# Optimization experiments

Hardware: AMD Instinct MI355X
Metric: run time of the kernel (lower is better)

The kernel has to match this reference:

```python
import jax, jax.numpy as jnp
import numpy as np

B, L, D = 32, 2048, 128
SCALE = 1.0 / float(np.sqrt(D))  # scale = 1/sqrt(dim_K) per docstring


def setup_inputs() -> dict:
    key = jax.random.key(0)
    kq, kk, kv, kb = jax.random.split(key, 4)
    return {
        "Q": jax.random.normal(kq, (B, L, D), dtype=jnp.float32),
        "K": jax.random.normal(kk, (B, L, D), dtype=jnp.float32),
        "V": jax.random.normal(kv, (B, L, D), dtype=jnp.float32),
        "bias": jax.random.normal(kb, (L, L), dtype=jnp.float32),
    }


def reference(Q, K, V, bias):
    # scores = Q @ K^T + bias (bias broadcast over batch), then scale, softmax, @ V
    scores = jnp.einsum("bqd,bkd->bqk", Q, K) + bias[None, :, :]
    attn = jax.nn.softmax(scores * SCALE, axis=-1)  # [B, L, L]
    context = jnp.einsum("bqk,bkd->bqd", attn, V)   # [B, L, D]
    return (context, attn[0])
```

## Files before the change

### kernel.cpp

```cpp
#include <hip/hip_runtime.h>
#include <cstdint>
#include <cstddef>

#define L_ 2048
#define D_ 128
#define B_ 32
#define NT_ 32

static constexpr float SCALE = 0.08838834764831845f;
static constexpr float LOG2E = 1.4426950408889634f;
static constexpr float THR_  = 8.0f;

typedef __bf16 bf16x8 __attribute__((ext_vector_type(8)));
typedef __bf16 bf16x4 __attribute__((ext_vector_type(4)));
typedef float  f32x4  __attribute__((ext_vector_type(4)));
typedef int    i32x4  __attribute__((ext_vector_type(4)));

typedef const __attribute__((address_space(1))) uint32_t* gas_t;
typedef __attribute__((address_space(3))) uint32_t*       las_t;

__device__ __forceinline__ void dma16(const void* g, void* l) {
  __builtin_amdgcn_global_load_lds((gas_t)g, (las_t)l, 16, 0, 0);
}

__global__ __launch_bounds__(256) void prep_kv(
    const float* __restrict__ K, const float* __restrict__ V,
    __bf16* __restrict__ gK, __bf16* __restrict__ gVt)
{
  const int b   = blockIdx.x >> 5;
  const int kt  = blockIdx.x & 31;
  const int tid = threadIdx.x;
  const size_t tile = ((size_t)b * NT_ + kt) * 8192;

#pragma unroll
  for (int i = 0; i < 4; ++i) {
    const int g  = tid + i * 256;
    const int r  = g >> 4;
    const int c  = g & 15;
    const int d0 = (c ^ (r & 7)) * 8;
    const float* src = K + ((size_t)b * L_ + kt * 64 + r) * D_ + d0;
    float4 a = *(const float4*)src;
    float4 e = *(const float4*)(src + 4);
    bf16x8 f;
    f[0]=(__bf16)a.x; f[1]=(__bf16)a.y; f[2]=(__bf16)a.z; f[3]=(__bf16)a.w;
    f[4]=(__bf16)e.x; f[5]=(__bf16)e.y; f[6]=(__bf16)e.z; f[7]=(__bf16)e.w;
    *(bf16x8*)((char*)(gK + tile) + r * 256 + c * 16) = f;
  }

  __shared__ alignas(16) __bf16 Vt[8192];
  char* vb = (char*)Vt;
  const int vr     = tid & 63;
  const int vdbase = (tid >> 6) * 32;
  const float* vrow = V + ((size_t)b * L_ + kt * 64 + vr) * D_ + vdbase;
#pragma unroll
  for (int c = 0; c < 8; ++c) {
    float4 v4 = *(const float4*)(vrow + c * 4);
    const int d0 = vdbase + c * 4;
    float vv[4] = {v4.x, v4.y, v4.z, v4.w};
#pragma unroll
    for (int jj = 0; jj < 4; ++jj) {
      const int d = d0 + jj;
      *(__bf16*)(vb + d * 128 + ((vr * 2) ^ ((d & 7) << 4))) = (__bf16)vv[jj];
    }
  }
  __syncthreads();
#pragma unroll
  for (int i = 0; i < 4; ++i) {
    const int off = (tid + i * 256) * 16;
    *(i32x4*)((char*)(gVt + tile) + off) = *(const i32x4*)(vb + off);
  }
}

__global__ __launch_bounds__(256) void prep_bias(
    const float* __restrict__ bias, float* __restrict__ biasS)
{
#pragma unroll
  for (int it = 0; it < 4; ++it) {
    const size_t idx = ((size_t)it * 1024 + blockIdx.x) * 256 + threadIdx.x;
    float4 v = ((const float4*)bias)[idx];
    v.x *= SCALE; v.y *= SCALE; v.z *= SCALE; v.w *= SCALE;
    ((float4*)biasS)[idx] = v;
  }
}

template<int MODE>
__global__ __launch_bounds__(512, 4) void attn_fwd(
    const float* __restrict__ Q, const float* __restrict__ K,
    const float* __restrict__ V, const float* __restrict__ bias,
    const float* __restrict__ biasS,
    const __bf16* __restrict__ gK, const __bf16* __restrict__ gVt,
    float* __restrict__ ctx, float* __restrict__ attn0)
{
  const int id   = blockIdx.x;
  const int idx  = id >> 3;
  const int b    = (id & 7) * 4 + (idx >> 4);
  const int qblk = idx & 15;

  const int tid  = threadIdx.x;
  const int wave = tid >> 6;
  const int lane = tid & 63;
  const int lg   = lane >> 4;
  const int lr   = lane & 15;

  const int qbase = qblk * 128 + wave * 16;

  __shared__ alignas(16) __bf16 Ksh[8192];
  __shared__ alignas(16) __bf16 Vtsh[8192];
  __shared__ alignas(16) __bf16 Psh[8][16 * 64];

  const char* kb = (const char*)Ksh;
  const char* vb = (const char*)Vtsh;
  char* const pw = (char*)&Psh[wave][0];

  bf16x8 qf[4];
  {
    const float* qrow = Q + ((size_t)b * L_ + (qbase + lr)) * D_;
#pragma unroll
    for (int kc = 0; kc < 4; ++kc) {
      const int d0 = kc * 32 + lg * 8;
      float4 a = *(const float4*)(qrow + d0);
      float4 c = *(const float4*)(qrow + d0 + 4);
      bf16x8 f;
      f[0] = (__bf16)(a.x * SCALE); f[1] = (__bf16)(a.y * SCALE);
      f[2] = (__bf16)(a.z * SCALE); f[3] = (__bf16)(a.w * SCALE);
      f[4] = (__bf16)(c.x * SCALE); f[5] = (__bf16)(c.y * SCALE);
      f[6] = (__bf16)(c.z * SCALE); f[7] = (__bf16)(c.w * SCALE);
      qf[kc] = f;
    }
  }

  f32x4 Oacc[8];
#pragma unroll
  for (int i = 0; i < 8; ++i) Oacc[i] = (f32x4){0.f, 0.f, 0.f, 0.f};
  float m_run = -3.0e38f;
  float lp    = 0.f;

  auto stage_dma = [&](int kt) {
    const char* gk = (const char*)(gK + ((size_t)b * NT_ + kt) * 8192);
    const char* gv = (const char*)(gVt + ((size_t)b * NT_ + kt) * 8192);
#pragma unroll
    for (int i = 0; i < 2; ++i) {
      const int off = (wave * 2 + i) * 1024;
      dma16(gk + off + lane * 16, (char*)Ksh + off);
      dma16(gv + off + lane * 16, (char*)Vtsh + off);
    }
  };

  if constexpr (MODE >= 1) stage_dma(0);

  const int sP = (lr & 3);

  for (int kt = 0; kt < NT_; ++kt) {
    const int kvbase = kt * 64;

    if constexpr (MODE == 0) {
#pragma unroll
      for (int it = 0; it < 4; ++it) {
        const int g  = tid + it * 512;
        const int r  = g >> 5;
        const int d0 = (g & 31) * 4;
        const size_t src = ((size_t)b * L_ + (kvbase + r)) * D_ + d0;
        float4 kv4 = *(const float4*)(K + src);
        bf16x4 k4 = {(__bf16)kv4.x, (__bf16)kv4.y, (__bf16)kv4.z, (__bf16)kv4.w};
        *(bf16x4*)((char*)Ksh + r * 256 + ((d0 * 2) ^ ((r & 7) << 4))) = k4;
      }
      {
        const int vr = tid & 63;
        const int vdbase = (tid >> 6) * 16;
        const float* vrow = V + ((size_t)b * L_ + (kvbase + vr)) * D_ + vdbase;
#pragma unroll
        for (int c = 0; c < 4; ++c) {
          float4 v4 = *(const float4*)(vrow + c * 4);
          const int d0 = vdbase + c * 4;
          float vv[4] = {v4.x, v4.y, v4.z, v4.w};
#pragma unroll
          for (int jj = 0; jj < 4; ++jj) {
            const int d = d0 + jj;
            *(__bf16*)((char*)Vtsh + d * 128 + ((vr * 2) ^ ((d & 7) << 4))) = (__bf16)vv[jj];
          }
        }
      }
    }
    __syncthreads();

    float4 bf4[4];
    {
      const float* bp = (MODE == 2 ? biasS : bias)
                        + (size_t)(qbase + lr) * L_ + kvbase + lg * 4;
#pragma unroll
      for (int t = 0; t < 4; ++t) bf4[t] = *(const float4*)(bp + t * 16);
    }

    f32x4 Sacc[4];
#pragma unroll
    for (int t = 0; t < 4; ++t) Sacc[t] = (f32x4){0.f, 0.f, 0.f, 0.f};
    __builtin_amdgcn_s_setprio(1);
#pragma unroll
    for (int t = 0; t < 4; ++t) {
      const int r   = t * 16 + lr;
      const int swz = (r & 7) << 4;
#pragma unroll
      for (int kc = 0; kc < 4; ++kc) {
        const int d0 = kc * 32 + lg * 8;
        bf16x8 kf = *(const bf16x8*)(kb + r * 256 + ((d0 * 2) ^ swz));
        Sacc[t] = __builtin_amdgcn_mfma_f32_16x16x32_bf16(kf, qf[kc], Sacc[t], 0, 0, 0);
      }
    }
    __builtin_amdgcn_s_setprio(0);

    float zz[4][4];
#pragma unroll
    for (int t = 0; t < 4; ++t) {
      if constexpr (MODE == 2) {
        zz[t][0] = Sacc[t][0] + bf4[t].x; zz[t][1] = Sacc[t][1] + bf4[t].y;
        zz[t][2] = Sacc[t][2] + bf4[t].z; zz[t][3] = Sacc[t][3] + bf4[t].w;
      } else {
        zz[t][0] = fmaf(bf4[t].x, SCALE, Sacc[t][0]);
        zz[t][1] = fmaf(bf4[t].y, SCALE, Sacc[t][1]);
        zz[t][2] = fmaf(bf4[t].z, SCALE, Sacc[t][2]);
        zz[t][3] = fmaf(bf4[t].w, SCALE, Sacc[t][3]);
      }
    }
    if (b == 0) {
      float* ap = attn0 + (size_t)(qbase + lr) * L_ + kvbase + lg * 4;
#pragma unroll
      for (int t = 0; t < 4; ++t)
        *(float4*)(ap + t * 16) = make_float4(zz[t][0], zz[t][1], zz[t][2], zz[t][3]);
    }

    float mt = fmaxf(fmaxf(fmaxf(zz[0][0], zz[0][1]), fmaxf(zz[0][2], zz[0][3])),
                     fmaxf(fmaxf(zz[1][0], zz[1][1]), fmaxf(zz[1][2], zz[1][3])));
    mt = fmaxf(mt, fmaxf(fmaxf(zz[2][0], zz[2][1]), fmaxf(zz[2][2], zz[2][3])));
    mt = fmaxf(mt, fmaxf(fmaxf(zz[3][0], zz[3][1]), fmaxf(zz[3][2], zz[3][3])));
    mt = fmaxf(mt, __shfl_xor(mt, 16));
    mt = fmaxf(mt, __shfl_xor(mt, 32));

    if (__any(mt > m_run + THR_)) {
      const float mnew = fmaxf(m_run, mt);
      const float corr = exp2f((m_run - mnew) * LOG2E);
      m_run = mnew;
      lp *= corr;
      float cR[4];
#pragma unroll
      for (int j = 0; j < 4; ++j)
        cR[j] = __shfl(corr, (lane & 0x30) | (lg * 4 + j));
#pragma unroll
      for (int dt = 0; dt < 8; ++dt) {
        Oacc[dt][0] *= cR[0]; Oacc[dt][1] *= cR[1];
        Oacc[dt][2] *= cR[2]; Oacc[dt][3] *= cR[3];
      }
    }

    const float mh = m_run * LOG2E;
#pragma unroll
    for (int t = 0; t < 4; ++t) {
      bf16x4 pb;
#pragma unroll
      for (int j = 0; j < 4; ++j) {
        const float p = exp2f(fmaf(zz[t][j], LOG2E, -mh));
        lp += p;
        pb[j] = (__bf16)p;
      }
      *(bf16x4*)(pw + lr * 128 + ((t ^ sP) << 5) + (lg << 3)) = pb;
    }

    __builtin_amdgcn_s_setprio(1);
#pragma unroll
    for (int kc2 = 0; kc2 < 2; ++kc2) {
      const int c0  = kc2 * 32;
      const int t_r = kc2 * 2 + (lg >> 1);
      bf16x8 pa = *(const bf16x8*)(pw + lr * 128 + ((t_r ^ sP) << 5) + ((lg & 1) << 4));
#pragma unroll
      for (int dt = 0; dt < 8; ++dt) {
        const int d = dt * 16 + lr;
        bf16x8 vf = *(const bf16x8*)(vb + d * 128 + (((c0 + lg * 8) * 2) ^ ((d & 7) << 4)));
        Oacc[dt] = __builtin_amdgcn_mfma_f32_16x16x32_bf16(pa, vf, Oacc[dt], 0, 0, 0);
      }
    }
    __builtin_amdgcn_s_setprio(0);

    __syncthreads();
    if constexpr (MODE >= 1) {
      if (kt + 1 < NT_) stage_dma(kt + 1);
    }
  }

  float ls = lp;
  ls += __shfl_xor(ls, 16);
  ls += __shfl_xor(ls, 32);
  const float linv = 1.f / ls;
  float invR[4];
#pragma unroll
  for (int j = 0; j < 4; ++j)
    invR[j] = __shfl(linv, (lane & 0x30) | (lg * 4 + j));
#pragma unroll
  for (int dt = 0; dt < 8; ++dt) {
    const int d = dt * 16 + lr;
#pragma unroll
    for (int j = 0; j < 4; ++j) {
      const int q = qbase + lg * 4 + j;
      ctx[((size_t)b * L_ + q) * D_ + d] = Oacc[dt][j] * invR[j];
    }
  }
}

__global__ __launch_bounds__(256) void softmax_rows(float* __restrict__ attn0)
{
  const int row  = blockIdx.x;
  float* p = attn0 + (size_t)row * L_;
  const int tid  = threadIdx.x;
  const int wave = tid >> 6;
  const int lane = tid & 63;
  __shared__ float red[8];

  float4 a = ((const float4*)p)[tid];
  float4 c = ((const float4*)p)[tid + 256];
  float v[8] = {a.x, a.y, a.z, a.w, c.x, c.y, c.z, c.w};

  float mx = v[0];
#pragma unroll
  for (int i = 1; i < 8; ++i) mx = fmaxf(mx, v[i]);
#pragma unroll
  for (int msk = 1; msk < 64; msk <<= 1) mx = fmaxf(mx, __shfl_xor(mx, msk));
  if (lane == 0) red[wave] = mx;
  __syncthreads();
  mx = fmaxf(fmaxf(red[0], red[1]), fmaxf(red[2], red[3]));

  float e[8];
  float s = 0.f;
#pragma unroll
  for (int i = 0; i < 8; ++i) { e[i] = exp2f((v[i] - mx) * LOG2E); s += e[i]; }
#pragma unroll
  for (int msk = 1; msk < 64; msk <<= 1) s += __shfl_xor(s, msk);
  if (lane == 0) red[4 + wave] = s;
  __syncthreads();
  s = red[4] + red[5] + red[6] + red[7];
  const float inv = 1.f / s;

  float4 o0 = {e[0] * inv, e[1] * inv, e[2] * inv, e[3] * inv};
  float4 o1 = {e[4] * inv, e[5] * inv, e[6] * inv, e[7] * inv};
  ((float4*)p)[tid]       = o0;
  ((float4*)p)[tid + 256] = o1;
}

extern "C" void kernel_launch(void* const* d_in, const int* in_sizes, int n_in,
                              void* d_out, int out_size, void* d_ws, size_t ws_size,
                              hipStream_t stream) {
  const float* Q    = (const float*)d_in[0];
  const float* K    = (const float*)d_in[1];
  const float* V    = (const float*)d_in[2];
  const float* bias = (const float*)d_in[3];
  float* ctx   = (float*)d_out;
  float* attn0 = ctx + (size_t)B_ * L_ * D_;

  const size_t kvElems  = (size_t)B_ * L_ * D_;
  const size_t needKV   = 2 * kvElems * sizeof(__bf16);
  const size_t needAll  = needKV + (size_t)L_ * L_ * sizeof(float);

  __bf16* gK    = (__bf16*)d_ws;
  __bf16* gVt   = gK + kvElems;
  float*  biasS = (float*)(gVt + kvElems);

  if (ws_size >= needAll) {
    prep_kv<<<dim3(B_ * NT_), 256, 0, stream>>>(K, V, gK, gVt);
    prep_bias<<<dim3(1024), 256, 0, stream>>>(bias, biasS);
    attn_fwd<2><<<dim3(512), 512, 0, stream>>>(Q, K, V, bias, biasS, gK, gVt, ctx, attn0);
  } else if (ws_size >= needKV) {
    prep_kv<<<dim3(B_ * NT_), 256, 0, stream>>>(K, V, gK, gVt);
    attn_fwd<1><<<dim3(512), 512, 0, stream>>>(Q, K, V, bias, nullptr, gK, gVt, ctx, attn0);
  } else {
    attn_fwd<0><<<dim3(512), 512, 0, stream>>>(Q, K, V, bias, nullptr, nullptr, nullptr, ctx, attn0);
  }
  softmax_rows<<<L_, 256, 0, stream>>>(attn0);
}
```

Before: 155.7 us.

## Double-buffer K/V tiles and keep P in registers via permuted V layout

Doubles the LDS K and V buffers so the DMA for tile kt+2 is issued while tile kt is computed, using an explicit vmcnt wait plus barrier instead of full syncs. It also drops the per-wave P shared-memory round trip: the softmax probabilities are packed straight into the MFMA A operand in registers, and a row permutation (cperm) applied to the transposed V layout makes the key order match. This removes LDS traffic and a sync on P, at the cost of double the K/V LDS footprint, which may lower occupancy. It also relies on the hand-written vmcnt count matching the number of DMAs in flight.

```diff
diff --git a/kernel.cpp b/kernel.cpp
--- a/kernel.cpp
+++ b/kernel.cpp
@@ -21,6 +21,11 @@
 
 __device__ __forceinline__ void dma16(const void* g, void* l) {
   __builtin_amdgcn_global_load_lds((gas_t)g, (las_t)l, 16, 0, 0);
+}
+
+__device__ __forceinline__ int cperm(int r) {
+  return (r & 32) | (((r >> 3) & 1) << 4) | (((r >> 2) & 1) << 3)
+       | (((r >> 4) & 1) << 2) | (r & 3);
 }
 
 __global__ __launch_bounds__(256) void prep_kv(
@@ -50,6 +55,7 @@
   __shared__ alignas(16) __bf16 Vt[8192];
   char* vb = (char*)Vt;
   const int vr     = tid & 63;
+  const int vc     = cperm(vr);
   const int vdbase = (tid >> 6) * 32;
   const float* vrow = V + ((size_t)b * L_ + kt * 64 + vr) * D_ + vdbase;
 #pragma unroll
@@ -60,7 +66,7 @@
 #pragma unroll
     for (int jj = 0; jj < 4; ++jj) {
       const int d = d0 + jj;
-      *(__bf16*)(vb + d * 128 + ((vr * 2) ^ ((d & 7) << 4))) = (__bf16)vv[jj];
+      *(__bf16*)(vb + d * 128 + ((vc * 2) ^ ((d & 7) << 4))) = (__bf16)vv[jj];
     }
   }
   __syncthreads();
@@ -104,13 +110,8 @@
 
   const int qbase = qblk * 128 + wave * 16;
 
-  __shared__ alignas(16) __bf16 Ksh[8192];
-  __shared__ alignas(16) __bf16 Vtsh[8192];
-  __shared__ alignas(16) __bf16 Psh[8][16 * 64];
-
-  const char* kb = (const char*)Ksh;
-  const char* vb = (const char*)Vtsh;
-  char* const pw = (char*)&Psh[wave][0];
+  __shared__ alignas(16) __bf16 Ksh[2 * 8192];
+  __shared__ alignas(16) __bf16 Vtsh[2 * 8192];
 
   bf16x8 qf[4];
   {
@@ -135,25 +136,33 @@
   float m_run = -3.0e38f;
   float lp    = 0.f;
 
-  auto stage_dma = [&](int kt) {
+  auto stage_dma = [&](int kt, int bufsel) {
     const char* gk = (const char*)(gK + ((size_t)b * NT_ + kt) * 8192);
     const char* gv = (const char*)(gVt + ((size_t)b * NT_ + kt) * 8192);
+    char* kdst = (char*)Ksh + bufsel * 16384;
+    char* vdst = (char*)Vtsh + bufsel * 16384;
 #pragma unroll
     for (int i = 0; i < 2; ++i) {
       const int off = (wave * 2 + i) * 1024;
-      dma16(gk + off + lane * 16, (char*)Ksh + off);
-      dma16(gv + off + lane * 16, (char*)Vtsh + off);
+      dma16(gk + off + lane * 16, kdst + off);
+      dma16(gv + off + lane * 16, vdst + off);
     }
   };
 
-  if constexpr (MODE >= 1) stage_dma(0);
-
-  const int sP = (lr & 3);
+  if constexpr (MODE >= 1) { stage_dma(0, 0); stage_dma(1, 1); }
 
   for (int kt = 0; kt < NT_; ++kt) {
     const int kvbase = kt * 64;
-
-    if constexpr (MODE == 0) {
+    const int cur = (MODE >= 1) ? (kt & 1) : 0;
+    const char* kb = (const char*)Ksh + cur * 16384;
+    const char* vb = (const char*)Vtsh + cur * 16384;
+
+    if constexpr (MODE >= 1) {
+      if (kt + 1 < NT_) asm volatile("s_waitcnt vmcnt(4)" ::: "memory");
+      else              asm volatile("s_waitcnt vmcnt(0)" ::: "memory");
+      __builtin_amdgcn_s_barrier();
+      __builtin_amdgcn_sched_barrier(0);
+    } else {
 #pragma unroll
       for (int it = 0; it < 4; ++it) {
         const int g  = tid + it * 512;
@@ -166,6 +175,7 @@
       }
       {
         const int vr = tid & 63;
+        const int vc = cperm(vr);
         const int vdbase = (tid >> 6) * 16;
         const float* vrow = V + ((size_t)b * L_ + (kvbase + vr)) * D_ + vdbase;
 #pragma unroll
@@ -176,12 +186,12 @@
 #pragma unroll
           for (int jj = 0; jj < 4; ++jj) {
             const int d = d0 + jj;
-            *(__bf16*)((char*)Vtsh + d * 128 + ((vr * 2) ^ ((d & 7) << 4))) = (__bf16)vv[jj];
+            *(__bf16*)((char*)Vtsh + d * 128 + ((vc * 2) ^ ((d & 7) << 4))) = (__bf16)vv[jj];
           }
         }
       }
-    }
-    __syncthreads();
+      __syncthreads();
+    }
 
     float4 bf4[4];
     {
@@ -251,25 +261,27 @@
       }
     }
 
+    bf16x4 pbf[4];
     const float mh = m_run * LOG2E;
 #pragma unroll
     for (int t = 0; t < 4; ++t) {
-      bf16x4 pb;
 #pragma unroll
       for (int j = 0; j < 4; ++j) {
         const float p = exp2f(fmaf(zz[t][j], LOG2E, -mh));
         lp += p;
-        pb[j] = (__bf16)p;
-      }
-      *(bf16x4*)(pw + lr * 128 + ((t ^ sP) << 5) + (lg << 3)) = pb;
+        pbf[t][j] = (__bf16)p;
+      }
     }
 
     __builtin_amdgcn_s_setprio(1);
 #pragma unroll
     for (int kc2 = 0; kc2 < 2; ++kc2) {
-      const int c0  = kc2 * 32;
-      const int t_r = kc2 * 2 + (lg >> 1);
-      bf16x8 pa = *(const bf16x8*)(pw + lr * 128 + ((t_r ^ sP) << 5) + ((lg & 1) << 4));
+      bf16x8 pa;
+      pa[0] = pbf[kc2 * 2][0];     pa[1] = pbf[kc2 * 2][1];
+      pa[2] = pbf[kc2 * 2][2];     pa[3] = pbf[kc2 * 2][3];
+      pa[4] = pbf[kc2 * 2 + 1][0]; pa[5] = pbf[kc2 * 2 + 1][1];
+      pa[6] = pbf[kc2 * 2 + 1][2]; pa[7] = pbf[kc2 * 2 + 1][3];
+      const int c0 = kc2 * 32;
 #pragma unroll
       for (int dt = 0; dt < 8; ++dt) {
         const int d = dt * 16 + lr;
@@ -279,9 +291,13 @@
     }
     __builtin_amdgcn_s_setprio(0);
 
-    __syncthreads();
     if constexpr (MODE >= 1) {
-      if (kt + 1 < NT_) stage_dma(kt + 1);
+      __builtin_amdgcn_sched_barrier(0);
+      __builtin_amdgcn_s_barrier();
+      __builtin_amdgcn_sched_barrier(0);
+      if (kt + 2 < NT_) stage_dma(kt + 2, cur);
+    } else {
+      __syncthreads();
     }
   }
 
```

After: 157.8 us. About the same (+1.3%).

## Feed P directly from registers via permuted V layout; drop bias prescale kernel

Applied to the files above, without the earlier changes.

Permutes the key-column order of the transposed V tile (in both prep_kv and the fallback path) so that the bf16 probabilities held in each lane's MFMA output registers already match the A-operand layout of the PV MFMA. This removes the per-wave LDS round trip for P: the shared-memory buffer, its stores and its reloads. The change also removes the separate prep_bias kernel and the prescaled-bias path, and folds the scale into an FMA on the raw bias inside the main loop. That saves one launch and a 16MB read and write of the bias, and frees some LDS, which could raise occupancy.

```diff
diff --git a/kernel.cpp b/kernel.cpp
--- a/kernel.cpp
+++ b/kernel.cpp
@@ -21,6 +21,11 @@
 
 __device__ __forceinline__ void dma16(const void* g, void* l) {
   __builtin_amdgcn_global_load_lds((gas_t)g, (las_t)l, 16, 0, 0);
+}
+
+__device__ __forceinline__ int cperm(int r) {
+  return (r & 32) | (((r >> 3) & 1) << 4) | (((r >> 2) & 1) << 3)
+       | (((r >> 4) & 1) << 2) | (r & 3);
 }
 
 __global__ __launch_bounds__(256) void prep_kv(
@@ -50,6 +55,7 @@
   __shared__ alignas(16) __bf16 Vt[8192];
   char* vb = (char*)Vt;
   const int vr     = tid & 63;
+  const int vc     = cperm(vr);
   const int vdbase = (tid >> 6) * 32;
   const float* vrow = V + ((size_t)b * L_ + kt * 64 + vr) * D_ + vdbase;
 #pragma unroll
@@ -60,7 +66,7 @@
 #pragma unroll
     for (int jj = 0; jj < 4; ++jj) {
       const int d = d0 + jj;
-      *(__bf16*)(vb + d * 128 + ((vr * 2) ^ ((d & 7) << 4))) = (__bf16)vv[jj];
+      *(__bf16*)(vb + d * 128 + ((vc * 2) ^ ((d & 7) << 4))) = (__bf16)vv[jj];
     }
   }
   __syncthreads();
@@ -68,18 +74,6 @@
   for (int i = 0; i < 4; ++i) {
     const int off = (tid + i * 256) * 16;
     *(i32x4*)((char*)(gVt + tile) + off) = *(const i32x4*)(vb + off);
-  }
-}
-
-__global__ __launch_bounds__(256) void prep_bias(
-    const float* __restrict__ bias, float* __restrict__ biasS)
-{
-#pragma unroll
-  for (int it = 0; it < 4; ++it) {
-    const size_t idx = ((size_t)it * 1024 + blockIdx.x) * 256 + threadIdx.x;
-    float4 v = ((const float4*)bias)[idx];
-    v.x *= SCALE; v.y *= SCALE; v.z *= SCALE; v.w *= SCALE;
-    ((float4*)biasS)[idx] = v;
   }
 }
 
@@ -87,7 +81,6 @@
 __global__ __launch_bounds__(512, 4) void attn_fwd(
     const float* __restrict__ Q, const float* __restrict__ K,
     const float* __restrict__ V, const float* __restrict__ bias,
-    const float* __restrict__ biasS,
     const __bf16* __restrict__ gK, const __bf16* __restrict__ gVt,
     float* __restrict__ ctx, float* __restrict__ attn0)
 {
@@ -106,11 +99,8 @@
 
   __shared__ alignas(16) __bf16 Ksh[8192];
   __shared__ alignas(16) __bf16 Vtsh[8192];
-  __shared__ alignas(16) __bf16 Psh[8][16 * 64];
-
   const char* kb = (const char*)Ksh;
   const char* vb = (const char*)Vtsh;
-  char* const pw = (char*)&Psh[wave][0];
 
   bf16x8 qf[4];
   {
@@ -148,8 +138,6 @@
 
   if constexpr (MODE >= 1) stage_dma(0);
 
-  const int sP = (lr & 3);
-
   for (int kt = 0; kt < NT_; ++kt) {
     const int kvbase = kt * 64;
 
@@ -166,6 +154,7 @@
       }
       {
         const int vr = tid & 63;
+        const int vc = cperm(vr);
         const int vdbase = (tid >> 6) * 16;
         const float* vrow = V + ((size_t)b * L_ + (kvbase + vr)) * D_ + vdbase;
 #pragma unroll
@@ -176,7 +165,7 @@
 #pragma unroll
           for (int jj = 0; jj < 4; ++jj) {
             const int d = d0 + jj;
-            *(__bf16*)((char*)Vtsh + d * 128 + ((vr * 2) ^ ((d & 7) << 4))) = (__bf16)vv[jj];
+            *(__bf16*)((char*)Vtsh + d * 128 + ((vc * 2) ^ ((d & 7) << 4))) = (__bf16)vv[jj];
           }
         }
       }
@@ -185,8 +174,7 @@
 
     float4 bf4[4];
     {
-      const float* bp = (MODE == 2 ? biasS : bias)
-                        + (size_t)(qbase + lr) * L_ + kvbase + lg * 4;
+      const float* bp = bias + (size_t)(qbase + lr) * L_ + kvbase + lg * 4;
 #pragma unroll
       for (int t = 0; t < 4; ++t) bf4[t] = *(const float4*)(bp + t * 16);
     }
@@ -211,15 +199,10 @@
     float zz[4][4];
 #pragma unroll
     for (int t = 0; t < 4; ++t) {
-      if constexpr (MODE == 2) {
-        zz[t][0] = Sacc[t][0] + bf4[t].x; zz[t][1] = Sacc[t][1] + bf4[t].y;
-        zz[t][2] = Sacc[t][2] + bf4[t].z; zz[t][3] = Sacc[t][3] + bf4[t].w;
-      } else {
-        zz[t][0] = fmaf(bf4[t].x, SCALE, Sacc[t][0]);
-        zz[t][1] = fmaf(bf4[t].y, SCALE, Sacc[t][1]);
-        zz[t][2] = fmaf(bf4[t].z, SCALE, Sacc[t][2]);
-        zz[t][3] = fmaf(bf4[t].w, SCALE, Sacc[t][3]);
-      }
+      zz[t][0] = fmaf(bf4[t].x, SCALE, Sacc[t][0]);
+      zz[t][1] = fmaf(bf4[t].y, SCALE, Sacc[t][1]);
+      zz[t][2] = fmaf(bf4[t].z, SCALE, Sacc[t][2]);
+      zz[t][3] = fmaf(bf4[t].w, SCALE, Sacc[t][3]);
     }
     if (b == 0) {
       float* ap = attn0 + (size_t)(qbase + lr) * L_ + kvbase + lg * 4;
@@ -251,25 +234,27 @@
       }
     }
 
+    bf16x4 pbf[4];
     const float mh = m_run * LOG2E;
 #pragma unroll
     for (int t = 0; t < 4; ++t) {
-      bf16x4 pb;
 #pragma unroll
       for (int j = 0; j < 4; ++j) {
         const float p = exp2f(fmaf(zz[t][j], LOG2E, -mh));
         lp += p;
-        pb[j] = (__bf16)p;
-      }
-      *(bf16x4*)(pw + lr * 128 + ((t ^ sP) << 5) + (lg << 3)) = pb;
+        pbf[t][j] = (__bf16)p;
+      }
     }
 
     __builtin_amdgcn_s_setprio(1);
 #pragma unroll
     for (int kc2 = 0; kc2 < 2; ++kc2) {
-      const int c0  = kc2 * 32;
-      const int t_r = kc2 * 2 + (lg >> 1);
-      bf16x8 pa = *(const bf16x8*)(pw + lr * 128 + ((t_r ^ sP) << 5) + ((lg & 1) << 4));
+      bf16x8 pa;
+      pa[0] = pbf[kc2 * 2][0];     pa[1] = pbf[kc2 * 2][1];
+      pa[2] = pbf[kc2 * 2][2];     pa[3] = pbf[kc2 * 2][3];
+      pa[4] = pbf[kc2 * 2 + 1][0]; pa[5] = pbf[kc2 * 2 + 1][1];
+      pa[6] = pbf[kc2 * 2 + 1][2]; pa[7] = pbf[kc2 * 2 + 1][3];
+      const int c0 = kc2 * 32;
 #pragma unroll
       for (int dt = 0; dt < 8; ++dt) {
         const int d = dt * 16 + lr;
@@ -353,23 +338,17 @@
   float* ctx   = (float*)d_out;
   float* attn0 = ctx + (size_t)B_ * L_ * D_;
 
-  const size_t kvElems  = (size_t)B_ * L_ * D_;
-  const size_t needKV   = 2 * kvElems * sizeof(__bf16);
-  const size_t needAll  = needKV + (size_t)L_ * L_ * sizeof(float);
-
-  __bf16* gK    = (__bf16*)d_ws;
-  __bf16* gVt   = gK + kvElems;
-  float*  biasS = (float*)(gVt + kvElems);
-
-  if (ws_size >= needAll) {
+  const size_t kvElems = (size_t)B_ * L_ * D_;
+  const size_t needKV  = 2 * kvElems * sizeof(__bf16);
+
+  __bf16* gK  = (__bf16*)d_ws;
+  __bf16* gVt = gK + kvElems;
+
+  if (ws_size >= needKV) {
     prep_kv<<<dim3(B_ * NT_), 256, 0, stream>>>(K, V, gK, gVt);
-    prep_bias<<<dim3(1024), 256, 0, stream>>>(bias, biasS);
-    attn_fwd<2><<<dim3(512), 512, 0, stream>>>(Q, K, V, bias, biasS, gK, gVt, ctx, attn0);
-  } else if (ws_size >= needKV) {
-    prep_kv<<<dim3(B_ * NT_), 256, 0, stream>>>(K, V, gK, gVt);
-    attn_fwd<1><<<dim3(512), 512, 0, stream>>>(Q, K, V, bias, nullptr, gK, gVt, ctx, attn0);
+    attn_fwd<1><<<dim3(512), 512, 0, stream>>>(Q, K, V, bias, gK, gVt, ctx, attn0);
   } else {
-    attn_fwd<0><<<dim3(512), 512, 0, stream>>>(Q, K, V, bias, nullptr, nullptr, nullptr, ctx, attn0);
+    attn_fwd<0><<<dim3(512), 512, 0, stream>>>(Q, K, V, bias, nullptr, nullptr, ctx, attn0);
   }
   softmax_rows<<<L_, 256, 0, stream>>>(attn0);
 }
```

Result: faster. 148.8 us (median of 2 runs) (-4.5%).
